# Performance work log

Measured on AMD Instinct MI355X. Metric: run time of the kernel, lower is better.

## Reference

```python
import jax, jax.numpy as jnp
import numpy as np

D_MODEL = 1024
NUM_HEADS = 16
DEPTH = D_MODEL // NUM_HEADS
B, S = 4, 2048


def setup_inputs() -> dict:
    key = jax.random.key(0)
    ks = jax.random.split(key, 13)
    sd = 1.0 / np.sqrt(D_MODEL)
    inp = {
        "q_in": jax.random.normal(ks[0], (B, S, D_MODEL), jnp.float32),
        "k_in": jax.random.normal(ks[1], (B, S, D_MODEL), jnp.float32),
        "v_in": jax.random.normal(ks[2], (B, S, D_MODEL), jnp.float32),
        # binary padding/causal-style mask: 1 = masked position
        "m_in": (jax.random.uniform(ks[3], (B, 1, S, S)) < 0.1).astype(jnp.float32),
        "Wq": jax.random.normal(ks[4], (D_MODEL, D_MODEL), jnp.float32) * sd,
        "bq": jax.random.normal(ks[5], (D_MODEL,), jnp.float32) * 0.01,
        "Wk": jax.random.normal(ks[6], (D_MODEL, D_MODEL), jnp.float32) * sd,
        "bk": jax.random.normal(ks[7], (D_MODEL,), jnp.float32) * 0.01,
        "Wv": jax.random.normal(ks[8], (D_MODEL, D_MODEL), jnp.float32) * sd,
        "bv": jax.random.normal(ks[9], (D_MODEL,), jnp.float32) * 0.01,
        "Wo": jax.random.normal(ks[10], (D_MODEL, D_MODEL), jnp.float32) * sd,
        "bo": jax.random.normal(ks[11], (D_MODEL,), jnp.float32) * 0.01,
    }
    return inp


def _split(t):
    # [B,S,D] -> [B,H,S,depth]
    b, s, _ = t.shape
    return t.reshape(b, s, NUM_HEADS, DEPTH).transpose(0, 2, 1, 3)


def reference(q_in, k_in, v_in, m_in, Wq, bq, Wk, bk, Wv, bv, Wo, bo):
    # torch Linear: x @ W^T + b
    q = _split(q_in @ Wq.T + bq)
    k = _split(k_in @ Wk.T + bk)
    v = _split(v_in @ Wv.T + bv)
    scale = jnp.sqrt(jnp.asarray(DEPTH, jnp.float32))
    scores = jnp.einsum("bhqd,bhkd->bhqk", q, k) / scale
    scores = scores - m_in * 1e6
    attn = jax.nn.softmax(scores, axis=-1)
    out = jnp.einsum("bhqk,bhkd->bhqd", attn, v)  # [B,H,S,depth]
    out = out.transpose(0, 2, 1, 3).reshape(q_in.shape[0], -1, D_MODEL)
    return out @ Wo.T + bo
```

## Files before the change

kernel.cpp:

```cpp
#include <hip/hip_runtime.h>


typedef __bf16 bf16_t;
typedef __bf16 bf16x4 __attribute__((ext_vector_type(4)));
typedef __bf16 bf16x8 __attribute__((ext_vector_type(8)));
typedef float floatx4 __attribute__((ext_vector_type(4)));

#define DMODEL 1024
#define NHEAD  16
#define DEPTH  64
#define BATCH  4
#define SEQ    2048
#define MROWS  (BATCH * SEQ)

#define QSCALE 0.18033688011112042f

#define GLDS16(gaddr, laddr)                                                   \
  __builtin_amdgcn_global_load_lds(                                            \
      (__attribute__((address_space(1))) void*)(gaddr),                        \
      (__attribute__((address_space(3))) void*)(laddr), 16, 0, 0)

__global__ __launch_bounds__(256) void cvt_weights(
    const float* __restrict__ w0, const float* __restrict__ w1,
    const float* __restrict__ w2, const float* __restrict__ w3,
    bf16_t* __restrict__ out) {
  const int n_per4 = (DMODEL * DMODEL) / 4;
  int idx = blockIdx.x * blockDim.x + threadIdx.x;
  int t = idx / n_per4;
  int e4 = idx - t * n_per4;
  const float* src = (t == 0) ? w0 : (t == 1) ? w1 : (t == 2) ? w2 : w3;
  const float sc = (t == 0) ? QSCALE : 1.0f;
  float4 v = ((const float4*)src)[e4];
  bf16_t* dst = out + (size_t)t * (DMODEL * DMODEL) + (size_t)e4 * 4;
  dst[0] = (bf16_t)(v.x * sc); dst[1] = (bf16_t)(v.y * sc);
  dst[2] = (bf16_t)(v.z * sc); dst[3] = (bf16_t)(v.w * sc);
}

__global__ __launch_bounds__(256) void cvt_one(
    const float* __restrict__ src, bf16_t* __restrict__ dst) {
  size_t i = (size_t)blockIdx.x * blockDim.x + threadIdx.x;
  const float4* s = (const float4*)(src + i * 8);
  float4 f0 = s[0], f1 = s[1];
  bf16x8 o;
  o[0] = (bf16_t)f0.x; o[1] = (bf16_t)f0.y; o[2] = (bf16_t)f0.z; o[3] = (bf16_t)f0.w;
  o[4] = (bf16_t)f1.x; o[5] = (bf16_t)f1.y; o[6] = (bf16_t)f1.z; o[7] = (bf16_t)f1.w;
  *(bf16x8*)(dst + i * 8) = o;
}

__global__ __launch_bounds__(256) void mask_prepack(
    const float* __restrict__ m, unsigned int* __restrict__ M32) {
  size_t t = (size_t)blockIdx.x * blockDim.x + threadIdx.x;
  int lane = t & 63;
  int it = (t >> 6) & 31;
  int g  = (t >> 11) & 63;
  int b  = (int)(t >> 17);
  int quad = lane >> 4, l16 = lane & 15;
  unsigned int bits = 0;
#pragma unroll
  for (int mi = 0; mi < 2; mi++) {
#pragma unroll
    for (int r = 0; r < 4; r++) {
      const int q = g * 32 + mi * 16 + quad * 4 + r;
      const float* row = m + ((size_t)b * SEQ + q) * SEQ + it * 64 + l16;
#pragma unroll
      for (int ni = 0; ni < 4; ni++) {
        if (row[ni * 16] == 0.f) bits |= 1u << ((mi * 4 + r) * 4 + ni);
      }
    }
  }
  M32[t] = bits;
}

template <int OMODE>
__global__ __launch_bounds__(256) void gemm128(
    const bf16_t* __restrict__ A, const bf16_t* __restrict__ Bt,
    const float* __restrict__ bias, float bias_scale, void* __restrict__ Ov,
    int M, int N, int K) {
  __shared__ __align__(16) bf16_t As[128 * 32];
  __shared__ __align__(16) bf16_t Bs[128 * 32];
  const int tid = threadIdx.x;
  const int lane = tid & 63;
  const int w = tid >> 6;
  const int quad = lane >> 4;
  const int l16 = lane & 15;
  const int wm = w & 1, wn = w >> 1;

  const int lin = blockIdx.x + 8 * blockIdx.y;
  const int c = lin & 7;
  const int j = lin >> 3;
  const int n0 = (j & 7) * 128;
  const int m0 = ((j >> 3) * 8 + c) * 128;

  const int r4 = lane >> 2;
  const int c4 = (lane & 3) ^ (r4 & 3);
  const bf16_t* Ag = A + (size_t)(m0 + w * 32 + r4) * K + c4 * 8;
  const bf16_t* Bg = Bt + (size_t)(n0 + w * 32 + r4) * K + c4 * 8;
  char* AsB = (char*)As + (w * 32) * 64;
  char* BsB = (char*)Bs + (w * 32) * 64;

  floatx4 acc[4][4] = {};

  for (int kk = 0; kk < K; kk += 32) {
    __syncthreads();
    GLDS16(Ag + kk, AsB);
    GLDS16(Ag + kk + (size_t)16 * K, AsB + 16 * 64);
    GLDS16(Bg + kk, BsB);
    GLDS16(Bg + kk + (size_t)16 * K, BsB + 16 * 64);
    __syncthreads();

    bf16x8 af[4], bfr[4];
#pragma unroll
    for (int mi = 0; mi < 4; mi++) {
      const char* Arow = (const char*)As + (wm * 64 + mi * 16 + l16) * 64;
      af[mi] = *(const bf16x8*)(Arow + ((quad ^ (l16 & 3)) * 16));
    }
#pragma unroll
    for (int ni = 0; ni < 4; ni++) {
      const char* Brow = (const char*)Bs + (wn * 64 + ni * 16 + l16) * 64;
      bfr[ni] = *(const bf16x8*)(Brow + ((quad ^ (l16 & 3)) * 16));
    }
#pragma unroll
    for (int mi = 0; mi < 4; mi++)
#pragma unroll
      for (int ni = 0; ni < 4; ni++)
        acc[mi][ni] = __builtin_amdgcn_mfma_f32_16x16x32_bf16(af[mi], bfr[ni], acc[mi][ni], 0, 0, 0);
  }

#pragma unroll
  for (int ni = 0; ni < 4; ni++) {
    const int col = n0 + wn * 64 + ni * 16 + l16;
    const float bv = bias_scale * bias[col];
#pragma unroll
    for (int mi = 0; mi < 4; mi++) {
#pragma unroll
      for (int r = 0; r < 4; r++) {
        const int row = m0 + wm * 64 + mi * 16 + quad * 4 + r;
        const float val = acc[mi][ni][r] + bv;
        if (OMODE == 0) {
          const int b = row >> 11, s = row & (SEQ - 1);
          const int h = col >> 6, d = col & (DEPTH - 1);
          ((bf16_t*)Ov)[((((size_t)b * NHEAD + h) * SEQ + s) << 6) + d] = (bf16_t)val;
        } else if (OMODE == 1) {
          const int b = row >> 11, s = row & (SEQ - 1);
          const int h = col >> 6, d = col & (DEPTH - 1);
          ((bf16_t*)Ov)[(((size_t)b * NHEAD + h) * DEPTH + d) * SEQ + s] = (bf16_t)val;
        } else {
          ((float*)Ov)[(size_t)row * N + col] = val;
        }
      }
    }
  }
}

__global__ __launch_bounds__(256) void attn_kernel(
    const bf16_t* __restrict__ Qh, const bf16_t* __restrict__ Kh,
    const bf16_t* __restrict__ Vt, const unsigned int* __restrict__ M32,
    bf16_t* __restrict__ O) {
  const int lane = threadIdx.x & 63;
  const int w = __builtin_amdgcn_readfirstlane(threadIdx.x >> 6);
  const int quad = lane >> 4;
  const int l16 = lane & 15;

  const int lin = blockIdx.x + 8 * (blockIdx.y + 16 * blockIdx.z);
  const int c = lin & 7;
  const int j = lin >> 3;
  const int p = (j & 7) * 8 + c;
  const int qt = j >> 3;
  const int h = p & 15;
  const int b = p >> 4;
  const int q0 = qt * 256;

  const bf16_t* Qb = Qh + ((size_t)b * NHEAD + h) * SEQ * DEPTH;
  const bf16_t* Kb = Kh + ((size_t)b * NHEAD + h) * SEQ * DEPTH;
  const bf16_t* Vb = Vt + ((size_t)b * NHEAD + h) * DEPTH * SEQ;
  const unsigned int* Mw0 =
      M32 + ((size_t)b * 64 + (qt * 8 + w * 2)) * 32 * 64 + lane;
  const unsigned int* Mw1 = Mw0 + 32 * 64;

  __shared__ __align__(16) bf16_t Ksm[64 * 64];
  __shared__ __align__(16) bf16_t Vsm[64 * 64];
  __shared__ __align__(16) bf16_t Pw[4][64][68];

  const int r8 = lane >> 3;
  const int c8 = (lane & 7) ^ r8;
  const bf16_t* Kg = Kb + (size_t)(w * 16 + r8) * DEPTH + c8 * 8;
  const bf16_t* Vg = Vb + (size_t)(w * 16 + r8) * SEQ + c8 * 8;
  char* KsB = (char*)Ksm + (w * 16) * 128;
  char* VsB = (char*)Vsm + (w * 16) * 128;

  bf16x8 aq[4][2];
#pragma unroll
  for (int mi = 0; mi < 4; mi++) {
    const bf16_t* qp = Qb + (size_t)(q0 + w * 64 + mi * 16 + l16) * DEPTH + quad * 8;
    aq[mi][0] = *(const bf16x8*)qp;
    aq[mi][1] = *(const bf16x8*)(qp + 32);
  }

  floatx4 acco[4][4] = {};
  float lsum[4][4] = {};
  const int swz = l16 & 7;

  for (int it = 0; it < SEQ / 64; ++it) {
    const int sk = it * 64;
    __syncthreads();
    GLDS16(Kg + (size_t)sk * DEPTH, KsB);
    GLDS16(Kg + (size_t)sk * DEPTH + 8 * DEPTH, KsB + 8 * 128);
    GLDS16(Vg + sk, VsB);
    GLDS16(Vg + sk + (size_t)8 * SEQ, VsB + 8 * 128);
    __syncthreads();

    const unsigned int mw0 = Mw0[it * 64];
    const unsigned int mw1 = Mw1[it * 64];

#pragma unroll
    for (int ni = 0; ni < 4; ni++) {
      const char* Krow = (const char*)Ksm + (ni * 16 + l16) * 128;
      bf16x8 k0 = *(const bf16x8*)(Krow + ((quad ^ swz) * 16));
      bf16x8 k1 = *(const bf16x8*)(Krow + (((4 + quad) ^ swz) * 16));
      floatx4 s[4];
#pragma unroll
      for (int mi = 0; mi < 4; mi++) {
        floatx4 z = {};
        z = __builtin_amdgcn_mfma_f32_16x16x32_bf16(aq[mi][0], k0, z, 0, 0, 0);
        s[mi] = __builtin_amdgcn_mfma_f32_16x16x32_bf16(aq[mi][1], k1, z, 0, 0, 0);
      }
#pragma unroll
      for (int mi = 0; mi < 4; mi++) {
        const unsigned int mword = (mi < 2) ? mw0 : mw1;
        const int mb = (mi & 1) * 16;
#pragma unroll
        for (int r = 0; r < 4; r++) {
          float pv = __builtin_amdgcn_exp2f(s[mi][r]);
          const int idx = mb + r * 4 + ni;
          const int km = ((int)(mword << (31 - idx))) >> 31;
          pv = __int_as_float(__float_as_int(pv) & km);
          lsum[mi][r] += pv;
          Pw[w][mi * 16 + quad * 4 + r][ni * 16 + l16] = (bf16_t)pv;
        }
      }
    }

    bf16x8 pa[4][2];
#pragma unroll
    for (int mi = 0; mi < 4; mi++) {
#pragma unroll
      for (int kb = 0; kb < 2; kb++) {
        const bf16_t* pp = &Pw[w][mi * 16 + l16][kb * 32 + quad * 8];
        bf16x4 lo = *(const bf16x4*)pp;
        bf16x4 hi = *(const bf16x4*)(pp + 4);
        pa[mi][kb] = __builtin_shufflevector(lo, hi, 0, 1, 2, 3, 4, 5, 6, 7);
      }
    }
#pragma unroll
    for (int ni = 0; ni < 4; ni++) {
      const char* Vrow = (const char*)Vsm + (ni * 16 + l16) * 128;
#pragma unroll
      for (int kb = 0; kb < 2; kb++) {
        bf16x8 vb = *(const bf16x8*)(Vrow + ((((kb * 4) + quad) ^ swz) * 16));
#pragma unroll
        for (int mi = 0; mi < 4; mi++)
          acco[mi][ni] = __builtin_amdgcn_mfma_f32_16x16x32_bf16(pa[mi][kb], vb, acco[mi][ni], 0, 0, 0);
      }
    }
  }

  float inv_l[4][4];
#pragma unroll
  for (int mi = 0; mi < 4; mi++)
#pragma unroll
    for (int r = 0; r < 4; r++) {
      float s = lsum[mi][r];
      s += __shfl_xor(s, 1);
      s += __shfl_xor(s, 2);
      s += __shfl_xor(s, 4);
      s += __shfl_xor(s, 8);
      inv_l[mi][r] = __frcp_rn(s);
    }

#pragma unroll
  for (int mi = 0; mi < 4; mi++)
#pragma unroll
    for (int ni = 0; ni < 4; ni++)
#pragma unroll
      for (int r = 0; r < 4; r++) {
        const int s = q0 + w * 64 + mi * 16 + quad * 4 + r;
        const int d = h * DEPTH + ni * 16 + l16;
        O[((size_t)b * SEQ + s) * DMODEL + d] = (bf16_t)(acco[mi][ni][r] * inv_l[mi][r]);
      }
}

extern "C" void kernel_launch(void* const* d_in, const int* in_sizes, int n_in,
                              void* d_out, int out_size, void* d_ws, size_t ws_size,
                              hipStream_t stream) {
  const float* q_in = (const float*)d_in[0];
  const float* k_in = (const float*)d_in[1];
  const float* v_in = (const float*)d_in[2];
  const float* m_in = (const float*)d_in[3];
  const float* Wq = (const float*)d_in[4];
  const float* bq = (const float*)d_in[5];
  const float* Wk = (const float*)d_in[6];
  const float* bk = (const float*)d_in[7];
  const float* Wv = (const float*)d_in[8];
  const float* bv = (const float*)d_in[9];
  const float* Wo = (const float*)d_in[10];
  const float* bo = (const float*)d_in[11];

  char* ws = (char*)d_ws;
  const size_t MB = 1024 * 1024;
  bf16_t* wbf = (bf16_t*)ws;
  bf16_t* Wq_bf = wbf + 0 * (size_t)DMODEL * DMODEL;
  bf16_t* Wk_bf = wbf + 1 * (size_t)DMODEL * DMODEL;
  bf16_t* Wv_bf = wbf + 2 * (size_t)DMODEL * DMODEL;
  bf16_t* Wo_bf = wbf + 3 * (size_t)DMODEL * DMODEL;
  bf16_t* Abf  = (bf16_t*)(ws + 8 * MB);
  bf16_t* Obuf = (bf16_t*)(ws + 8 * MB);
  bf16_t* Qh   = (bf16_t*)(ws + 24 * MB);
  bf16_t* Kh   = (bf16_t*)(ws + 40 * MB);
  bf16_t* Vth  = (bf16_t*)(ws + 56 * MB);
  unsigned int* M32 = (unsigned int*)(ws + 72 * MB);

  cvt_weights<<<(4 * (DMODEL * DMODEL / 4)) / 256, 256, 0, stream>>>(
      Wq, Wk, Wv, Wo, wbf);
  mask_prepack<<<(BATCH * 64 * 32 * 64) / 256, 256, 0, stream>>>(m_in, M32);

  dim3 gg(DMODEL / 128, MROWS / 128);
  const int cvt_blocks = (MROWS * DMODEL / 8) / 256;

  cvt_one<<<cvt_blocks, 256, 0, stream>>>(q_in, Abf);
  gemm128<0><<<gg, 256, 0, stream>>>(Abf, Wq_bf, bq, QSCALE, Qh, MROWS, DMODEL, DMODEL);
  cvt_one<<<cvt_blocks, 256, 0, stream>>>(k_in, Abf);
  gemm128<0><<<gg, 256, 0, stream>>>(Abf, Wk_bf, bk, 1.0f, Kh, MROWS, DMODEL, DMODEL);
  cvt_one<<<cvt_blocks, 256, 0, stream>>>(v_in, Abf);
  gemm128<1><<<gg, 256, 0, stream>>>(Abf, Wv_bf, bv, 1.0f, Vth, MROWS, DMODEL, DMODEL);

  dim3 ga(SEQ / 256, NHEAD, BATCH);
  attn_kernel<<<ga, 256, 0, stream>>>(Qh, Kh, Vth, M32, Obuf);

  gemm128<2><<<gg, 256, 0, stream>>>(Obuf, Wo_bf, bo, 1.0f, d_out, MROWS, DMODEL, DMODEL);
}
```

Baseline: 497.0 us.

## Batch QKV projections into one launch and halve attention query tile

Merges the three input conversions into a single kernel and the three Q/K/V projection GEMMs into one launch that selects its weights, bias and output layout from blockIdx.z. This gives each launch three times as many blocks and removes per-launch overhead. The attention kernel now gives each block 128 query rows (32 per wave) instead of 256, doubling the grid to 1024 blocks and cutting register pressure, which should raise occupancy. In exchange, each K/V tile loaded into shared memory is reused by fewer queries, so K/V traffic doubles, and the workspace grows to hold all three converted inputs.

Result: faster. 438.6 us (-11.8%).

```diff
diff --git a/kernel.cpp b/kernel.cpp
--- a/kernel.cpp
+++ b/kernel.cpp
@@ -36,10 +36,15 @@
   dst[2] = (bf16_t)(v.z * sc); dst[3] = (bf16_t)(v.w * sc);
 }
 
-__global__ __launch_bounds__(256) void cvt_one(
-    const float* __restrict__ src, bf16_t* __restrict__ dst) {
+__global__ __launch_bounds__(256) void cvt3(
+    const float* __restrict__ q, const float* __restrict__ k,
+    const float* __restrict__ v, bf16_t* __restrict__ dst) {
+  const size_t n8 = (size_t)MROWS * DMODEL / 8;
   size_t i = (size_t)blockIdx.x * blockDim.x + threadIdx.x;
-  const float4* s = (const float4*)(src + i * 8);
+  int t = (int)(i / n8);
+  size_t e = i - (size_t)t * n8;
+  const float* src = (t == 0) ? q : (t == 1) ? k : v;
+  const float4* s = (const float4*)(src + e * 8);
   float4 f0 = s[0], f1 = s[1];
   bf16x8 o;
   o[0] = (bf16_t)f0.x; o[1] = (bf16_t)f0.y; o[2] = (bf16_t)f0.z; o[3] = (bf16_t)f0.w;
@@ -71,10 +76,94 @@
   M32[t] = bits;
 }
 
-template <int OMODE>
-__global__ __launch_bounds__(256) void gemm128(
+__global__ __launch_bounds__(256) void gemm_qkv(
+    const bf16_t* __restrict__ Abf3, const bf16_t* __restrict__ Wbf,
+    const float* __restrict__ bq, const float* __restrict__ bk,
+    const float* __restrict__ bv, bf16_t* __restrict__ Qh,
+    bf16_t* __restrict__ Kh, bf16_t* __restrict__ Vth) {
+  __shared__ __align__(16) bf16_t As[128 * 32];
+  __shared__ __align__(16) bf16_t Bs[128 * 32];
+  const int K = DMODEL;
+  const int tid = threadIdx.x;
+  const int lane = tid & 63;
+  const int w = tid >> 6;
+  const int quad = lane >> 4;
+  const int l16 = lane & 15;
+  const int wm = w & 1, wn = w >> 1;
+  const int z = blockIdx.z;
+
+  const bf16_t* A = Abf3 + (size_t)z * MROWS * DMODEL;
+  const bf16_t* Bt = Wbf + (size_t)z * DMODEL * DMODEL;
+  const float* bias = (z == 0) ? bq : (z == 1) ? bk : bv;
+  const float bias_scale = (z == 0) ? QSCALE : 1.0f;
+  bf16_t* Ov = (z == 0) ? Qh : (z == 1) ? Kh : Vth;
+
+  const int lin = blockIdx.x + 8 * blockIdx.y;
+  const int c = lin & 7;
+  const int j = lin >> 3;
+  const int n0 = (j & 7) * 128;
+  const int m0 = ((j >> 3) * 8 + c) * 128;
+
+  const int r4 = lane >> 2;
+  const int c4 = (lane & 3) ^ (r4 & 3);
+  const bf16_t* Ag = A + (size_t)(m0 + w * 32 + r4) * K + c4 * 8;
+  const bf16_t* Bg = Bt + (size_t)(n0 + w * 32 + r4) * K + c4 * 8;
+  char* AsB = (char*)As + (w * 32) * 64;
+  char* BsB = (char*)Bs + (w * 32) * 64;
+
+  floatx4 acc[4][4] = {};
+
+  for (int kk = 0; kk < K; kk += 32) {
+    __syncthreads();
+    GLDS16(Ag + kk, AsB);
+    GLDS16(Ag + kk + (size_t)16 * K, AsB + 16 * 64);
+    GLDS16(Bg + kk, BsB);
+    GLDS16(Bg + kk + (size_t)16 * K, BsB + 16 * 64);
+    __syncthreads();
+
+    bf16x8 af[4], bfr[4];
+#pragma unroll
+    for (int mi = 0; mi < 4; mi++) {
+      const char* Arow = (const char*)As + (wm * 64 + mi * 16 + l16) * 64;
+      af[mi] = *(const bf16x8*)(Arow + ((quad ^ (l16 & 3)) * 16));
+    }
+#pragma unroll
+    for (int ni = 0; ni < 4; ni++) {
+      const char* Brow = (const char*)Bs + (wn * 64 + ni * 16 + l16) * 64;
+      bfr[ni] = *(const bf16x8*)(Brow + ((quad ^ (l16 & 3)) * 16));
+    }
+#pragma unroll
+    for (int mi = 0; mi < 4; mi++)
+#pragma unroll
+      for (int ni = 0; ni < 4; ni++)
+        acc[mi][ni] = __builtin_amdgcn_mfma_f32_16x16x32_bf16(af[mi], bfr[ni], acc[mi][ni], 0, 0, 0);
+  }
+
+#pragma unroll
+  for (int ni = 0; ni < 4; ni++) {
+    const int col = n0 + wn * 64 + ni * 16 + l16;
+    const float bvl = bias_scale * bias[col];
+    const int hh = col >> 6, d = col & (DEPTH - 1);
+#pragma unroll
+    for (int mi = 0; mi < 4; mi++) {
+#pragma unroll
+      for (int r = 0; r < 4; r++) {
+        const int row = m0 + wm * 64 + mi * 16 + quad * 4 + r;
+        const float val = acc[mi][ni][r] + bvl;
+        const int bb = row >> 11, s = row & (SEQ - 1);
+        if (z != 2) {
+          Ov[((((size_t)bb * NHEAD + hh) * SEQ + s) << 6) + d] = (bf16_t)val;
+        } else {
+          Ov[(((size_t)bb * NHEAD + hh) * DEPTH + d) * SEQ + s] = (bf16_t)val;
+        }
+      }
+    }
+  }
+}
+
+__global__ __launch_bounds__(256) void gemm_wo(
     const bf16_t* __restrict__ A, const bf16_t* __restrict__ Bt,
-    const float* __restrict__ bias, float bias_scale, void* __restrict__ Ov,
+    const float* __restrict__ bias, float* __restrict__ Ov,
     int M, int N, int K) {
   __shared__ __align__(16) bf16_t As[128 * 32];
   __shared__ __align__(16) bf16_t Bs[128 * 32];
@@ -129,26 +218,14 @@
 #pragma unroll
   for (int ni = 0; ni < 4; ni++) {
     const int col = n0 + wn * 64 + ni * 16 + l16;
-    const float bv = bias_scale * bias[col];
-#pragma unroll
-    for (int mi = 0; mi < 4; mi++) {
+    const float bv = bias[col];
+#pragma unroll
+    for (int mi = 0; mi < 4; mi++)
 #pragma unroll
       for (int r = 0; r < 4; r++) {
         const int row = m0 + wm * 64 + mi * 16 + quad * 4 + r;
-        const float val = acc[mi][ni][r] + bv;
-        if (OMODE == 0) {
-          const int b = row >> 11, s = row & (SEQ - 1);
-          const int h = col >> 6, d = col & (DEPTH - 1);
-          ((bf16_t*)Ov)[((((size_t)b * NHEAD + h) * SEQ + s) << 6) + d] = (bf16_t)val;
-        } else if (OMODE == 1) {
-          const int b = row >> 11, s = row & (SEQ - 1);
-          const int h = col >> 6, d = col & (DEPTH - 1);
-          ((bf16_t*)Ov)[(((size_t)b * NHEAD + h) * DEPTH + d) * SEQ + s] = (bf16_t)val;
-        } else {
-          ((float*)Ov)[(size_t)row * N + col] = val;
-        }
-      }
-    }
+        Ov[(size_t)row * N + col] = acc[mi][ni][r] + bv;
+      }
   }
 }
 
@@ -161,25 +238,24 @@
   const int quad = lane >> 4;
   const int l16 = lane & 15;
 
-  const int lin = blockIdx.x + 8 * (blockIdx.y + 16 * blockIdx.z);
-  const int c = lin & 7;
-  const int j = lin >> 3;
-  const int p = (j & 7) * 8 + c;
-  const int qt = j >> 3;
+  const int lin = blockIdx.x + 16 * blockIdx.y + 256 * blockIdx.z;
+  const int x8 = lin & 7;
+  const int kk = lin >> 3;
+  const int qt = kk & 15;
+  const int p = ((kk >> 4) << 3) | x8;
   const int h = p & 15;
   const int b = p >> 4;
-  const int q0 = qt * 256;
+  const int q0 = qt * 128;
 
   const bf16_t* Qb = Qh + ((size_t)b * NHEAD + h) * SEQ * DEPTH;
   const bf16_t* Kb = Kh + ((size_t)b * NHEAD + h) * SEQ * DEPTH;
   const bf16_t* Vb = Vt + ((size_t)b * NHEAD + h) * DEPTH * SEQ;
-  const unsigned int* Mw0 =
-      M32 + ((size_t)b * 64 + (qt * 8 + w * 2)) * 32 * 64 + lane;
-  const unsigned int* Mw1 = Mw0 + 32 * 64;
+  const unsigned int* Mw =
+      M32 + ((size_t)b * 64 + (qt * 4 + w)) * 32 * 64 + lane;
 
   __shared__ __align__(16) bf16_t Ksm[64 * 64];
   __shared__ __align__(16) bf16_t Vsm[64 * 64];
-  __shared__ __align__(16) bf16_t Pw[4][64][68];
+  __shared__ __align__(16) bf16_t Pw[4][32][68];
 
   const int r8 = lane >> 3;
   const int c8 = (lane & 7) ^ r8;
@@ -188,16 +264,16 @@
   char* KsB = (char*)Ksm + (w * 16) * 128;
   char* VsB = (char*)Vsm + (w * 16) * 128;
 
-  bf16x8 aq[4][2];
-#pragma unroll
-  for (int mi = 0; mi < 4; mi++) {
-    const bf16_t* qp = Qb + (size_t)(q0 + w * 64 + mi * 16 + l16) * DEPTH + quad * 8;
+  bf16x8 aq[2][2];
+#pragma unroll
+  for (int mi = 0; mi < 2; mi++) {
+    const bf16_t* qp = Qb + (size_t)(q0 + w * 32 + mi * 16 + l16) * DEPTH + quad * 8;
     aq[mi][0] = *(const bf16x8*)qp;
     aq[mi][1] = *(const bf16x8*)(qp + 32);
   }
 
-  floatx4 acco[4][4] = {};
-  float lsum[4][4] = {};
+  floatx4 acco[2][4] = {};
+  float lsum[2][4] = {};
   const int swz = l16 & 7;
 
   for (int it = 0; it < SEQ / 64; ++it) {
@@ -209,29 +285,26 @@
     GLDS16(Vg + sk + (size_t)8 * SEQ, VsB + 8 * 128);
     __syncthreads();
 
-    const unsigned int mw0 = Mw0[it * 64];
-    const unsigned int mw1 = Mw1[it * 64];
+    const unsigned int mword = Mw[it * 64];
 
 #pragma unroll
     for (int ni = 0; ni < 4; ni++) {
       const char* Krow = (const char*)Ksm + (ni * 16 + l16) * 128;
       bf16x8 k0 = *(const bf16x8*)(Krow + ((quad ^ swz) * 16));
       bf16x8 k1 = *(const bf16x8*)(Krow + (((4 + quad) ^ swz) * 16));
-      floatx4 s[4];
-#pragma unroll
-      for (int mi = 0; mi < 4; mi++) {
+      floatx4 s[2];
+#pragma unroll
+      for (int mi = 0; mi < 2; mi++) {
         floatx4 z = {};
         z = __builtin_amdgcn_mfma_f32_16x16x32_bf16(aq[mi][0], k0, z, 0, 0, 0);
         s[mi] = __builtin_amdgcn_mfma_f32_16x16x32_bf16(aq[mi][1], k1, z, 0, 0, 0);
       }
 #pragma unroll
-      for (int mi = 0; mi < 4; mi++) {
-        const unsigned int mword = (mi < 2) ? mw0 : mw1;
-        const int mb = (mi & 1) * 16;
+      for (int mi = 0; mi < 2; mi++) {
 #pragma unroll
         for (int r = 0; r < 4; r++) {
           float pv = __builtin_amdgcn_exp2f(s[mi][r]);
-          const int idx = mb + r * 4 + ni;
+          const int idx = (mi * 4 + r) * 4 + ni;
           const int km = ((int)(mword << (31 - idx))) >> 31;
           pv = __int_as_float(__float_as_int(pv) & km);
           lsum[mi][r] += pv;
@@ -240,9 +313,9 @@
       }
     }
 
-    bf16x8 pa[4][2];
-#pragma unroll
-    for (int mi = 0; mi < 4; mi++) {
+    bf16x8 pa[2][2];
+#pragma unroll
+    for (int mi = 0; mi < 2; mi++) {
 #pragma unroll
       for (int kb = 0; kb < 2; kb++) {
         const bf16_t* pp = &Pw[w][mi * 16 + l16][kb * 32 + quad * 8];
@@ -258,15 +331,15 @@
       for (int kb = 0; kb < 2; kb++) {
         bf16x8 vb = *(const bf16x8*)(Vrow + ((((kb * 4) + quad) ^ swz) * 16));
 #pragma unroll
-        for (int mi = 0; mi < 4; mi++)
+        for (int mi = 0; mi < 2; mi++)
           acco[mi][ni] = __builtin_amdgcn_mfma_f32_16x16x32_bf16(pa[mi][kb], vb, acco[mi][ni], 0, 0, 0);
       }
     }
   }
 
-  float inv_l[4][4];
-#pragma unroll
-  for (int mi = 0; mi < 4; mi++)
+  float inv_l[2][4];
+#pragma unroll
+  for (int mi = 0; mi < 2; mi++)
 #pragma unroll
     for (int r = 0; r < 4; r++) {
       float s = lsum[mi][r];
@@ -278,12 +351,12 @@
     }
 
 #pragma unroll
-  for (int mi = 0; mi < 4; mi++)
+  for (int mi = 0; mi < 2; mi++)
 #pragma unroll
     for (int ni = 0; ni < 4; ni++)
 #pragma unroll
       for (int r = 0; r < 4; r++) {
-        const int s = q0 + w * 64 + mi * 16 + quad * 4 + r;
+        const int s = q0 + w * 32 + mi * 16 + quad * 4 + r;
         const int d = h * DEPTH + ni * 16 + l16;
         O[((size_t)b * SEQ + s) * DMODEL + d] = (bf16_t)(acco[mi][ni][r] * inv_l[mi][r]);
       }
@@ -307,34 +380,28 @@
 
   char* ws = (char*)d_ws;
   const size_t MB = 1024 * 1024;
-  bf16_t* wbf = (bf16_t*)ws;
-  bf16_t* Wq_bf = wbf + 0 * (size_t)DMODEL * DMODEL;
-  bf16_t* Wk_bf = wbf + 1 * (size_t)DMODEL * DMODEL;
-  bf16_t* Wv_bf = wbf + 2 * (size_t)DMODEL * DMODEL;
-  bf16_t* Wo_bf = wbf + 3 * (size_t)DMODEL * DMODEL;
-  bf16_t* Abf  = (bf16_t*)(ws + 8 * MB);
+  bf16_t* wbf  = (bf16_t*)ws;
+  bf16_t* Abf3 = (bf16_t*)(ws + 8 * MB);
   bf16_t* Obuf = (bf16_t*)(ws + 8 * MB);
-  bf16_t* Qh   = (bf16_t*)(ws + 24 * MB);
-  bf16_t* Kh   = (bf16_t*)(ws + 40 * MB);
-  bf16_t* Vth  = (bf16_t*)(ws + 56 * MB);
-  unsigned int* M32 = (unsigned int*)(ws + 72 * MB);
+  bf16_t* Qh   = (bf16_t*)(ws + 56 * MB);
+  bf16_t* Kh   = (bf16_t*)(ws + 72 * MB);
+  bf16_t* Vth  = (bf16_t*)(ws + 88 * MB);
+  unsigned int* M32 = (unsigned int*)(ws + 104 * MB);
 
   cvt_weights<<<(4 * (DMODEL * DMODEL / 4)) / 256, 256, 0, stream>>>(
       Wq, Wk, Wv, Wo, wbf);
+  cvt3<<<(3 * (MROWS * DMODEL / 8)) / 256, 256, 0, stream>>>(
+      q_in, k_in, v_in, Abf3);
   mask_prepack<<<(BATCH * 64 * 32 * 64) / 256, 256, 0, stream>>>(m_in, M32);
 
-  dim3 gg(DMODEL / 128, MROWS / 128);
-  const int cvt_blocks = (MROWS * DMODEL / 8) / 256;
-
-  cvt_one<<<cvt_blocks, 256, 0, stream>>>(q_in, Abf);
-  gemm128<0><<<gg, 256, 0, stream>>>(Abf, Wq_bf, bq, QSCALE, Qh, MROWS, DMODEL, DMODEL);
-  cvt_one<<<cvt_blocks, 256, 0, stream>>>(k_in, Abf);
-  gemm128<0><<<gg, 256, 0, stream>>>(Abf, Wk_bf, bk, 1.0f, Kh, MROWS, DMODEL, DMODEL);
-  cvt_one<<<cvt_blocks, 256, 0, stream>>>(v_in, Abf);
-  gemm128<1><<<gg, 256, 0, stream>>>(Abf, Wv_bf, bv, 1.0f, Vth, MROWS, DMODEL, DMODEL);
-
-  dim3 ga(SEQ / 256, NHEAD, BATCH);
+  dim3 gqkv(8, 64, 3);
+  gemm_qkv<<<gqkv, 256, 0, stream>>>(Abf3, wbf, bq, bk, bv, Qh, Kh, Vth);
+
+  dim3 ga(SEQ / 128, NHEAD, BATCH);
   attn_kernel<<<ga, 256, 0, stream>>>(Qh, Kh, Vth, M32, Obuf);
 
-  gemm128<2><<<gg, 256, 0, stream>>>(Obuf, Wo_bf, bo, 1.0f, d_out, MROWS, DMODEL, DMODEL);
-}
+  dim3 gg(8, 64);
+  gemm_wo<<<gg, 256, 0, stream>>>(
+      Obuf, wbf + 3 * (size_t)DMODEL * DMODEL, bo, (float*)d_out,
+      MROWS, DMODEL, DMODEL);
+}
```
